# Performance work log

Measured on AMD Instinct MI355X. Metric: run time of the kernel, lower is better.

## Reference

```python
import jax, jax.numpy as jnp
import numpy as np

B, T, I, H = 128, 512, 512, 512


def setup_inputs() -> dict:
    key = jax.random.key(0)
    k1, k2, k3, k4, k5 = jax.random.split(key, 5)
    scale_x = 1.0 / np.sqrt(I)
    scale_h = 1.0 / np.sqrt(H)
    return {
        "x": jax.random.normal(k1, (B, T, I), dtype=jnp.float32),
        "h0": jax.random.normal(k2, (B, H), dtype=jnp.float32),
        "Wx": jax.random.normal(k3, (3 * H, I), dtype=jnp.float32) * scale_x,
        "bx": jax.random.normal(k4, (3 * H,), dtype=jnp.float32) * scale_x,
        "Wh": jax.random.normal(k5, (3 * H, H), dtype=jnp.float32) * scale_h,
    }


def reference(x, h0, Wx, bx, Wh):
    # Precompute input projections for all timesteps as one big GEMM:
    # [B,T,I] @ [I,3H] -> [B,T,3H]
    x_lin = jnp.einsum('bti,ki->btk', x, Wx) + bx
    x_lin_t = jnp.swapaxes(x_lin, 0, 1)  # [T,B,3H] time-major for scan

    def step(h, xl):
        h_lin = h @ Wh.T                          # [B,3H]
        x_z, x_r, x_n = jnp.split(xl, 3, axis=1)
        h_z, h_r, h_n = jnp.split(h_lin, 3, axis=1)
        z = jax.nn.sigmoid(x_z + h_z)
        r = jax.nn.sigmoid(x_r + h_r)
        n = jnp.tanh(x_n + r * h_n)
        h_new = (1.0 - z) * n + z * h
        return h_new, h_new

    h_final, ys = jax.lax.scan(step, h0, x_lin_t)  # ys: [T,B,H]
    y = jnp.swapaxes(ys, 0, 1)                      # [B,T,H]
    return (y, h_final)
```

## Files before the change

### kernel.cpp

```cpp
#include <hip/hip_runtime.h>
#include <hip/hip_bf16.h>

#define B_  128
#define T_  512
#define HID 512
#define NG  1536
#define CSTRIDE 16

#define GCNT(t)  ((t)*CSTRIDE)
#define FLAG0    (T_*CSTRIDE)
#define MEM0     (FLAG0 + 256*CSTRIDE)
#define INIT0    (MEM0 + 8*CSTRIDE)
#define SYNC_U32 (INIT0 + CSTRIDE)

typedef __attribute__((ext_vector_type(8))) short bf16x8;
typedef __attribute__((ext_vector_type(4))) float f32x4;
typedef unsigned int uint;
typedef unsigned short u16;

#define HROW 1024
#define HPAR 131072

__device__ __forceinline__ float bf2f(unsigned short h) {
  union { unsigned u; float f; } c; c.u = ((unsigned)h) << 16; return c.f;
}
__device__ __forceinline__ unsigned short f2bf_rn(float f) {
  union { float f; unsigned u; } c; c.f = f;
  return (unsigned short)((c.u + 0x7FFFu + ((c.u >> 16) & 1u)) >> 16);
}
__device__ __forceinline__ void split1(float f, short& hi, short& lo) {
  union { float f; unsigned u; } c; c.f = f;
  unsigned short h = (unsigned short)(c.u >> 16);
  float r = f - bf2f(h);
  hi = (short)h; lo = (short)f2bf_rn(r);
}
__device__ __forceinline__ void split8(float4 a, float4 b, bf16x8& hi, bf16x8& lo) {
  float v[8] = {a.x,a.y,a.z,a.w,b.x,b.y,b.z,b.w};
  #pragma unroll
  for (int i = 0; i < 8; ++i) { short h,l; split1(v[i],h,l); hi[i]=h; lo[i]=l; }
}

__device__ __forceinline__ uint aload_rlx(const uint* p) {
  return __hip_atomic_load(p, __ATOMIC_RELAXED, __HIP_MEMORY_SCOPE_AGENT);
}

__global__ void h0_pack(const float* __restrict__ h0, u16* __restrict__ hbuf) {
  int i = blockIdx.x * 256 + threadIdx.x;
  short hi, lo; split1(h0[i], hi, lo);
  u16* p = hbuf + HPAR + (i >> 9) * HROW + (i & 511);
  p[0]   = (u16)hi;
  p[512] = (u16)lo;
}

template<bool WSF32>
__global__ __launch_bounds__(256) void xlin_kernel(const float* __restrict__ x,
                                                   const float* __restrict__ Wx,
                                                   const float* __restrict__ bx,
                                                   void* __restrict__ xlin) {
  const int lane = threadIdx.x & 63;
  const int w    = threadIdx.x >> 6;
  const int wm   = w & 1, wn = w >> 1;
  const int quad = lane >> 4, l16 = lane & 15;
  const long m0  = (long)blockIdx.y * 128;
  const int  n0  = blockIdx.x * 128;

  f32x4 acc[4][4];
  #pragma unroll
  for (int i = 0; i < 4; ++i)
    #pragma unroll
    for (int j = 0; j < 4; ++j) acc[i][j] = (f32x4){0.f,0.f,0.f,0.f};

  for (int kk = 0; kk < 16; ++kk) {
    const int kq = kk*32 + quad*8;
    bf16x8 ahi[4], alo[4], bhi[4], blo[4];
    #pragma unroll
    for (int i = 0; i < 4; ++i) {
      const float* p = x + (m0 + wm*64 + i*16 + l16) * HID + kq;
      float4 f0 = ((const float4*)p)[0], f1 = ((const float4*)p)[1];
      split8(f0, f1, ahi[i], alo[i]);
      const float* q = Wx + (long)(n0 + wn*64 + i*16 + l16) * HID + kq;
      float4 g0 = ((const float4*)q)[0], g1 = ((const float4*)q)[1];
      split8(g0, g1, bhi[i], blo[i]);
    }
    #pragma unroll
    for (int i = 0; i < 4; ++i)
      #pragma unroll
      for (int j = 0; j < 4; ++j) {
        acc[i][j] = __builtin_amdgcn_mfma_f32_16x16x32_bf16(ahi[i], bhi[j], acc[i][j], 0, 0, 0);
        acc[i][j] = __builtin_amdgcn_mfma_f32_16x16x32_bf16(ahi[i], blo[j], acc[i][j], 0, 0, 0);
        acc[i][j] = __builtin_amdgcn_mfma_f32_16x16x32_bf16(alo[i], bhi[j], acc[i][j], 0, 0, 0);
      }
  }
  #pragma unroll
  for (int i = 0; i < 4; ++i) {
    #pragma unroll
    for (int j = 0; j < 4; ++j) {
      const int n = n0 + wn*64 + j*16 + l16;
      const float bias = bx[n];
      #pragma unroll
      for (int r = 0; r < 4; ++r) {
        const long m = m0 + wm*64 + i*16 + quad*4 + r;
        const float v = acc[i][j][r] + bias;
        if (WSF32) ((float*)xlin)[m * NG + n] = v;
        else       ((unsigned short*)xlin)[m * NG + n] = f2bf_rn(v);
      }
    }
  }
}

template<bool WSF32>
__global__ __launch_bounds__(256, 1) void gru_rec(const void* __restrict__ xlin,
                                                  const float* __restrict__ Wh,
                                                  u16* __restrict__ hbuf,
                                                  uint* __restrict__ sync,
                                                  float* __restrict__ out) {
  __shared__ float red[3][4][16][17];
  __shared__ int sh_xcd, sh_cb, sh_kc;
  __shared__ uint sh_fast;
  const int tid  = threadIdx.x;
  const int lane = tid & 63;
  const int w    = tid >> 6;
  const int quad = lane >> 4, l16 = lane & 15;

  if (tid == 0) {
    uint id;
    __asm__ volatile("s_getreg_b32 %0, hwreg(HW_REG_XCC_ID, 0, 32)" : "=s"(id));
    const int xcd = (int)(id & 7u);
    uint xr = __hip_atomic_fetch_add(&sync[MEM0 + xcd*CSTRIDE], 1u,
                                     __ATOMIC_RELAXED, __HIP_MEMORY_SCOPE_AGENT);
    uint* ic = &sync[INIT0];
    uint gr = __hip_atomic_fetch_add(ic, 1u, __ATOMIC_ACQ_REL, __HIP_MEMORY_SCOPE_AGENT);
    while (aload_rlx(ic) < 256u) __builtin_amdgcn_s_sleep(1);
    (void)__hip_atomic_load(ic, __ATOMIC_ACQUIRE, __HIP_MEMORY_SCOPE_AGENT);
    bool bal = true;
    #pragma unroll
    for (int x = 0; x < 8; ++x)
      bal = bal && (aload_rlx(&sync[MEM0 + x*CSTRIDE]) == 32u);
    sh_xcd  = xcd;
    sh_fast = bal ? 1u : 0u;
    sh_cb   = bal ? xcd     : (int)(gr >> 5);
    sh_kc   = bal ? (int)xr : (int)(gr & 31u);
  }
  __syncthreads();
  const int  xcd   = sh_xcd;
  const bool fastm = (sh_fast != 0u);
  const int  cb    = sh_cb;
  const int  kc    = sh_kc;

  bf16x8 Bhi[3][4], Blo[3][4];
  #pragma unroll
  for (int g = 0; g < 3; ++g)
    #pragma unroll
    for (int kk = 0; kk < 4; ++kk) {
      const float* p = Wh + (long)(g*HID + kc*16 + l16) * HID + w*128 + kk*32 + quad*8;
      float4 f0 = ((const float4*)p)[0], f1 = ((const float4*)p)[1];
      split8(f0, f1, Bhi[g][kk], Blo[g][kk]);
    }

  const int bb   = tid >> 4;
  const int kk_  = tid & 15;
  const int brow = cb*16 + bb;
  const int ncol = kc*16 + kk_;
  float* yout = out;
  float* hfin = out + (long)B_ * T_ * HID;

  const int fragoff = (cb*16 + l16)*HROW + w*128 + quad*8;
  const int hpoff   = brow*HROW + ncol;

  float xq[8][3];
  float yq[8];

  {
    const long base = (long)brow * T_;
    #pragma unroll
    for (int q = 0; q < 8; ++q) {
      if (WSF32) {
        const float* xp = (const float*)xlin + (base + q) * NG + ncol;
        xq[q][0] = xp[0]; xq[q][1] = xp[HID]; xq[q][2] = xp[2*HID];
      } else {
        const unsigned short* xp = (const unsigned short*)xlin + (base + q) * NG + ncol;
        xq[q][0] = bf2f(xp[0]); xq[q][1] = bf2f(xp[HID]); xq[q][2] = bf2f(xp[2*HID]);
      }
    }
  }

  for (int tb = 0; tb < T_/8; ++tb) {
    #pragma unroll
    for (int ts = 0; ts < 8; ++ts) {
      const int t = tb*8 + ts;
      const float xz = xq[ts][0], xr = xq[ts][1], xn = xq[ts][2];

      if (t > 0) {
        if (fastm) {
          const uint* fp = &sync[FLAG0 + (xcd*32 + (lane & 31))*CSTRIDE];
          while (!__all(aload_rlx(fp) >= (uint)t)) __builtin_amdgcn_s_sleep(1);
        } else {
          if (tid == 0) {
            uint* gp = &sync[GCNT(t-1)];
            while (aload_rlx(gp) < 256u) __builtin_amdgcn_s_sleep(1);
            (void)__hip_atomic_load(gp, __ATOMIC_ACQUIRE, __HIP_MEMORY_SCOPE_AGENT);
          }
          __syncthreads();
        }
      }

      const u16* rb = hbuf + ((t + 1) & 1) * HPAR;
      u16*       wb = hbuf + (t & 1)       * HPAR;

      const u16* hp_ = rb + fragoff;
      const u16* hpp = rb + hpoff;
      uint4 u0,u1,u2,u3,u4,u5,u6,u7; uint hu, lu;
      asm volatile(
        "global_load_dwordx4 %0, %10, off sc0\n\t"
        "global_load_dwordx4 %1, %10, off offset:64 sc0\n\t"
        "global_load_dwordx4 %2, %10, off offset:128 sc0\n\t"
        "global_load_dwordx4 %3, %10, off offset:192 sc0\n\t"
        "global_load_dwordx4 %4, %10, off offset:1024 sc0\n\t"
        "global_load_dwordx4 %5, %10, off offset:1088 sc0\n\t"
        "global_load_dwordx4 %6, %10, off offset:1152 sc0\n\t"
        "global_load_dwordx4 %7, %10, off offset:1216 sc0\n\t"
        "global_load_ushort %8, %11, off sc0\n\t"
        "global_load_ushort %9, %11, off offset:1024 sc0\n\t"
        "s_waitcnt vmcnt(0)"
        : "=&v"(u0), "=&v"(u1), "=&v"(u2), "=&v"(u3),
          "=&v"(u4), "=&v"(u5), "=&v"(u6), "=&v"(u7),
          "=&v"(hu), "=&v"(lu)
        : "v"(hp_), "v"(hpp)
        : "memory");

      f32x4 acc[3] = { (f32x4){0,0,0,0}, (f32x4){0,0,0,0}, (f32x4){0,0,0,0} };
      {
        const bf16x8 ah0 = *(const bf16x8*)&u0, al0 = *(const bf16x8*)&u4;
        const bf16x8 ah1 = *(const bf16x8*)&u1, al1 = *(const bf16x8*)&u5;
        const bf16x8 ah2 = *(const bf16x8*)&u2, al2 = *(const bf16x8*)&u6;
        const bf16x8 ah3 = *(const bf16x8*)&u3, al3 = *(const bf16x8*)&u7;
        const bf16x8 AH[4] = {ah0, ah1, ah2, ah3};
        const bf16x8 AL[4] = {al0, al1, al2, al3};
        #pragma unroll
        for (int kk = 0; kk < 4; ++kk) {
          #pragma unroll
          for (int g = 0; g < 3; ++g) {
            acc[g] = __builtin_amdgcn_mfma_f32_16x16x32_bf16(AH[kk], Bhi[g][kk], acc[g], 0, 0, 0);
            acc[g] = __builtin_amdgcn_mfma_f32_16x16x32_bf16(AH[kk], Blo[g][kk], acc[g], 0, 0, 0);
            acc[g] = __builtin_amdgcn_mfma_f32_16x16x32_bf16(AL[kk], Bhi[g][kk], acc[g], 0, 0, 0);
          }
        }
      }
      #pragma unroll
      for (int g = 0; g < 3; ++g)
        #pragma unroll
        for (int r = 0; r < 4; ++r)
          red[g][w][quad*4 + r][l16] = acc[g][r];

      const float hp = bf2f((unsigned short)hu) + bf2f((unsigned short)lu);

      __syncthreads();

      float az = 0.f, ar = 0.f, an = 0.f;
      #pragma unroll
      for (int ww = 0; ww < 4; ++ww) {
        az += red[0][ww][bb][kk_];
        ar += red[1][ww][bb][kk_];
        an += red[2][ww][bb][kk_];
      }
      const float z = 1.f / (1.f + __expf(-(az + xz)));
      const float r = 1.f / (1.f + __expf(-(ar + xr)));
      const float pre = xn + r * an;
      const float e2 = __expf(-2.f * pre);
      const float n = 2.f / (1.f + e2) - 1.f;
      const float hn = (1.f - z) * n + z * hp;
      yq[ts] = hn;

      if (t < T_ - 1) {
        short shi, slo; split1(hn, shi, slo);
        u16* wp = wb + hpoff;
        wp[0]   = (u16)shi;
        wp[512] = (u16)slo;
      } else {
        hfin[brow*HID + ncol] = hn;
      }

      __syncthreads();
      if (t < T_ - 1) {
        if (fastm) {
          if (tid == 0)
            sync[FLAG0 + (xcd*32 + kc)*CSTRIDE] = (uint)(t + 1);
        } else {
          if (tid == 0)
            __hip_atomic_fetch_add(&sync[GCNT(t)], 1u,
                                   __ATOMIC_RELEASE, __HIP_MEMORY_SCOPE_AGENT);
        }
      }

      if (ts == 7) {
        #pragma unroll
        for (int q = 0; q < 8; ++q)
          __builtin_nontemporal_store(yq[q],
              &yout[((long)brow * T_ + tb*8 + q) * HID + ncol]);
        if (tb + 1 < T_/8) {
          const long base = (long)brow * T_ + (tb + 1)*8;
          #pragma unroll
          for (int q = 0; q < 8; ++q) {
            if (WSF32) {
              const float* xp = (const float*)xlin + (base + q) * NG + ncol;
              xq[q][0] = xp[0]; xq[q][1] = xp[HID]; xq[q][2] = xp[2*HID];
            } else {
              const unsigned short* xp = (const unsigned short*)xlin + (base + q) * NG + ncol;
              xq[q][0] = bf2f(xp[0]); xq[q][1] = bf2f(xp[HID]); xq[q][2] = bf2f(xp[2*HID]);
            }
          }
        }
      }
    }
  }
}

extern "C" void kernel_launch(void* const* d_in, const int* in_sizes, int n_in,
                              void* d_out, int out_size, void* d_ws, size_t ws_size,
                              hipStream_t stream) {
  const float* x  = (const float*)d_in[0];
  const float* h0 = (const float*)d_in[1];
  const float* Wx = (const float*)d_in[2];
  const float* bx = (const float*)d_in[3];
  const float* Wh = (const float*)d_in[4];
  float* out = (float*)d_out;

  const size_t xlin_f32  = (size_t)B_ * T_ * NG * 4;
  const size_t xlin_bf16 = (size_t)B_ * T_ * NG * 2;
  const size_t hbuf_sz   = (size_t)2 * HPAR * 2;
  const size_t sync_sz   = (size_t)SYNC_U32 * 4;

  const bool wsf32 = (ws_size >= xlin_f32 + hbuf_sz + sync_sz);
  const size_t xsz = wsf32 ? xlin_f32 : xlin_bf16;
  void* xlin = d_ws;
  u16*  hbuf = (u16*)((char*)d_ws + xsz);
  uint* sync = (uint*)((char*)d_ws + xsz + hbuf_sz);

  hipMemsetAsync(sync, 0, sync_sz, stream);
  h0_pack<<<256, 256, 0, stream>>>(h0, hbuf);
  if (wsf32) {
    xlin_kernel<true ><<<dim3(12, 512), 256, 0, stream>>>(x, Wx, bx, xlin);
    gru_rec<true >    <<<256, 256, 0, stream>>>(xlin, Wh, hbuf, sync, out);
  } else {
    xlin_kernel<false><<<dim3(12, 512), 256, 0, stream>>>(x, Wx, bx, xlin);
    gru_rec<false>    <<<256, 256, 0, stream>>>(xlin, Wh, hbuf, sync, out);
  }
}
```

Measured before the change: 2.022 ms.

## Halve recurrent workgroups, each computing 32 hidden columns, spin without sleep

The persistent recurrent kernel now launches 128 workgroups instead of 256. Each one handles 32 hidden columns per batch tile instead of 16, holding twice as many Wh fragments in registers and issuing twice the MFMAs per step. Fewer participants means the per-step flag barrier waits on fewer producers, which is meant to cut synchronisation latency. The fast-path spin loop also drops s_sleep to poll more aggressively. The trade-off is more serial MFMA and gate work per workgroup per timestep, higher register pressure, and half the CUs left idle.

```diff
diff --git a/kernel.cpp b/kernel.cpp
--- a/kernel.cpp
+++ b/kernel.cpp
@@ -12,6 +12,9 @@
 #define MEM0     (FLAG0 + 256*CSTRIDE)
 #define INIT0    (MEM0 + 8*CSTRIDE)
 #define SYNC_U32 (INIT0 + CSTRIDE)
+
+#define NWG      128
+#define NWG_XCD  16
 
 typedef __attribute__((ext_vector_type(8))) short bf16x8;
 typedef __attribute__((ext_vector_type(4))) float f32x4;
@@ -114,7 +117,7 @@
                                                   u16* __restrict__ hbuf,
                                                   uint* __restrict__ sync,
                                                   float* __restrict__ out) {
-  __shared__ float red[3][4][16][17];
+  __shared__ float red[3][4][16][34];
   __shared__ int sh_xcd, sh_cb, sh_kc;
   __shared__ uint sh_fast;
   const int tid  = threadIdx.x;
@@ -130,16 +133,16 @@
                                      __ATOMIC_RELAXED, __HIP_MEMORY_SCOPE_AGENT);
     uint* ic = &sync[INIT0];
     uint gr = __hip_atomic_fetch_add(ic, 1u, __ATOMIC_ACQ_REL, __HIP_MEMORY_SCOPE_AGENT);
-    while (aload_rlx(ic) < 256u) __builtin_amdgcn_s_sleep(1);
+    while (aload_rlx(ic) < (uint)NWG) __builtin_amdgcn_s_sleep(1);
     (void)__hip_atomic_load(ic, __ATOMIC_ACQUIRE, __HIP_MEMORY_SCOPE_AGENT);
     bool bal = true;
     #pragma unroll
     for (int x = 0; x < 8; ++x)
-      bal = bal && (aload_rlx(&sync[MEM0 + x*CSTRIDE]) == 32u);
+      bal = bal && (aload_rlx(&sync[MEM0 + x*CSTRIDE]) == (uint)NWG_XCD);
     sh_xcd  = xcd;
     sh_fast = bal ? 1u : 0u;
-    sh_cb   = bal ? xcd     : (int)(gr >> 5);
-    sh_kc   = bal ? (int)xr : (int)(gr & 31u);
+    sh_cb   = bal ? xcd     : (int)(gr >> 4);
+    sh_kc   = bal ? (int)xr : (int)(gr & 15u);
   }
   __syncthreads();
   const int  xcd   = sh_xcd;
@@ -147,39 +150,43 @@
   const int  cb    = sh_cb;
   const int  kc    = sh_kc;
 
-  bf16x8 Bhi[3][4], Blo[3][4];
+  bf16x8 Bhi[3][2][4], Blo[3][2][4];
   #pragma unroll
   for (int g = 0; g < 3; ++g)
     #pragma unroll
-    for (int kk = 0; kk < 4; ++kk) {
-      const float* p = Wh + (long)(g*HID + kc*16 + l16) * HID + w*128 + kk*32 + quad*8;
-      float4 f0 = ((const float4*)p)[0], f1 = ((const float4*)p)[1];
-      split8(f0, f1, Bhi[g][kk], Blo[g][kk]);
-    }
-
-  const int bb   = tid >> 4;
-  const int kk_  = tid & 15;
-  const int brow = cb*16 + bb;
-  const int ncol = kc*16 + kk_;
+    for (int c = 0; c < 2; ++c)
+      #pragma unroll
+      for (int kk = 0; kk < 4; ++kk) {
+        const float* p = Wh + (long)(g*HID + kc*32 + c*16 + l16) * HID + w*128 + kk*32 + quad*8;
+        float4 f0 = ((const float4*)p)[0], f1 = ((const float4*)p)[1];
+        split8(f0, f1, Bhi[g][c][kk], Blo[g][c][kk]);
+      }
+
+  const int bb    = tid >> 4;
+  const int kk2   = tid & 15;
+  const int brow  = cb*16 + bb;
+  const int ncol0 = kc*32 + kk2;
   float* yout = out;
   float* hfin = out + (long)B_ * T_ * HID;
 
   const int fragoff = (cb*16 + l16)*HROW + w*128 + quad*8;
-  const int hpoff   = brow*HROW + ncol;
-
-  float xq[8][3];
-  float yq[8];
+  const int hpoff   = brow*HROW + ncol0;
+
+  float xq[8][6];
+  float yq[8][2];
 
   {
     const long base = (long)brow * T_;
     #pragma unroll
     for (int q = 0; q < 8; ++q) {
       if (WSF32) {
-        const float* xp = (const float*)xlin + (base + q) * NG + ncol;
-        xq[q][0] = xp[0]; xq[q][1] = xp[HID]; xq[q][2] = xp[2*HID];
+        const float* xp = (const float*)xlin + (base + q) * NG + ncol0;
+        xq[q][0] = xp[0];  xq[q][1] = xp[HID];    xq[q][2] = xp[2*HID];
+        xq[q][3] = xp[16]; xq[q][4] = xp[HID+16]; xq[q][5] = xp[2*HID+16];
       } else {
-        const unsigned short* xp = (const unsigned short*)xlin + (base + q) * NG + ncol;
-        xq[q][0] = bf2f(xp[0]); xq[q][1] = bf2f(xp[HID]); xq[q][2] = bf2f(xp[2*HID]);
+        const unsigned short* xp = (const unsigned short*)xlin + (base + q) * NG + ncol0;
+        xq[q][0] = bf2f(xp[0]);  xq[q][1] = bf2f(xp[HID]);    xq[q][2] = bf2f(xp[2*HID]);
+        xq[q][3] = bf2f(xp[16]); xq[q][4] = bf2f(xp[HID+16]); xq[q][5] = bf2f(xp[2*HID+16]);
       }
     }
   }
@@ -188,16 +195,15 @@
     #pragma unroll
     for (int ts = 0; ts < 8; ++ts) {
       const int t = tb*8 + ts;
-      const float xz = xq[ts][0], xr = xq[ts][1], xn = xq[ts][2];
 
       if (t > 0) {
         if (fastm) {
-          const uint* fp = &sync[FLAG0 + (xcd*32 + (lane & 31))*CSTRIDE];
-          while (!__all(aload_rlx(fp) >= (uint)t)) __builtin_amdgcn_s_sleep(1);
+          const uint* fp = &sync[FLAG0 + (xcd*16 + (lane & 15))*CSTRIDE];
+          while (!__all(aload_rlx(fp) >= (uint)t)) { }
         } else {
           if (tid == 0) {
             uint* gp = &sync[GCNT(t-1)];
-            while (aload_rlx(gp) < 256u) __builtin_amdgcn_s_sleep(1);
+            while (aload_rlx(gp) < (uint)NWG) __builtin_amdgcn_s_sleep(1);
             (void)__hip_atomic_load(gp, __ATOMIC_ACQUIRE, __HIP_MEMORY_SCOPE_AGENT);
           }
           __syncthreads();
@@ -209,82 +215,97 @@
 
       const u16* hp_ = rb + fragoff;
       const u16* hpp = rb + hpoff;
-      uint4 u0,u1,u2,u3,u4,u5,u6,u7; uint hu, lu;
+      uint4 u0,u1,u2,u3,u4,u5,u6,u7; uint hu0, hu1, lu0, lu1;
       asm volatile(
-        "global_load_dwordx4 %0, %10, off sc0\n\t"
-        "global_load_dwordx4 %1, %10, off offset:64 sc0\n\t"
-        "global_load_dwordx4 %2, %10, off offset:128 sc0\n\t"
-        "global_load_dwordx4 %3, %10, off offset:192 sc0\n\t"
-        "global_load_dwordx4 %4, %10, off offset:1024 sc0\n\t"
-        "global_load_dwordx4 %5, %10, off offset:1088 sc0\n\t"
-        "global_load_dwordx4 %6, %10, off offset:1152 sc0\n\t"
-        "global_load_dwordx4 %7, %10, off offset:1216 sc0\n\t"
-        "global_load_ushort %8, %11, off sc0\n\t"
-        "global_load_ushort %9, %11, off offset:1024 sc0\n\t"
+        "global_load_dwordx4 %0, %12, off sc0\n\t"
+        "global_load_dwordx4 %1, %12, off offset:64 sc0\n\t"
+        "global_load_dwordx4 %2, %12, off offset:128 sc0\n\t"
+        "global_load_dwordx4 %3, %12, off offset:192 sc0\n\t"
+        "global_load_dwordx4 %4, %12, off offset:1024 sc0\n\t"
+        "global_load_dwordx4 %5, %12, off offset:1088 sc0\n\t"
+        "global_load_dwordx4 %6, %12, off offset:1152 sc0\n\t"
+        "global_load_dwordx4 %7, %12, off offset:1216 sc0\n\t"
+        "global_load_ushort %8, %13, off sc0\n\t"
+        "global_load_ushort %9, %13, off offset:32 sc0\n\t"
+        "global_load_ushort %10, %13, off offset:1024 sc0\n\t"
+        "global_load_ushort %11, %13, off offset:1056 sc0\n\t"
         "s_waitcnt vmcnt(0)"
         : "=&v"(u0), "=&v"(u1), "=&v"(u2), "=&v"(u3),
           "=&v"(u4), "=&v"(u5), "=&v"(u6), "=&v"(u7),
-          "=&v"(hu), "=&v"(lu)
+          "=&v"(hu0), "=&v"(hu1), "=&v"(lu0), "=&v"(lu1)
         : "v"(hp_), "v"(hpp)
         : "memory");
 
-      f32x4 acc[3] = { (f32x4){0,0,0,0}, (f32x4){0,0,0,0}, (f32x4){0,0,0,0} };
+      f32x4 acc[3][2];
+      #pragma unroll
+      for (int g = 0; g < 3; ++g)
+        #pragma unroll
+        for (int c = 0; c < 2; ++c) acc[g][c] = (f32x4){0,0,0,0};
       {
-        const bf16x8 ah0 = *(const bf16x8*)&u0, al0 = *(const bf16x8*)&u4;
-        const bf16x8 ah1 = *(const bf16x8*)&u1, al1 = *(const bf16x8*)&u5;
-        const bf16x8 ah2 = *(const bf16x8*)&u2, al2 = *(const bf16x8*)&u6;
-        const bf16x8 ah3 = *(const bf16x8*)&u3, al3 = *(const bf16x8*)&u7;
-        const bf16x8 AH[4] = {ah0, ah1, ah2, ah3};
-        const bf16x8 AL[4] = {al0, al1, al2, al3};
+        const bf16x8 AH[4] = { *(const bf16x8*)&u0, *(const bf16x8*)&u1,
+                               *(const bf16x8*)&u2, *(const bf16x8*)&u3 };
+        const bf16x8 AL[4] = { *(const bf16x8*)&u4, *(const bf16x8*)&u5,
+                               *(const bf16x8*)&u6, *(const bf16x8*)&u7 };
         #pragma unroll
         for (int kk = 0; kk < 4; ++kk) {
           #pragma unroll
           for (int g = 0; g < 3; ++g) {
-            acc[g] = __builtin_amdgcn_mfma_f32_16x16x32_bf16(AH[kk], Bhi[g][kk], acc[g], 0, 0, 0);
-            acc[g] = __builtin_amdgcn_mfma_f32_16x16x32_bf16(AH[kk], Blo[g][kk], acc[g], 0, 0, 0);
-            acc[g] = __builtin_amdgcn_mfma_f32_16x16x32_bf16(AL[kk], Bhi[g][kk], acc[g], 0, 0, 0);
+            #pragma unroll
+            for (int c = 0; c < 2; ++c) {
+              acc[g][c] = __builtin_amdgcn_mfma_f32_16x16x32_bf16(AH[kk], Bhi[g][c][kk], acc[g][c], 0, 0, 0);
+              acc[g][c] = __builtin_amdgcn_mfma_f32_16x16x32_bf16(AH[kk], Blo[g][c][kk], acc[g][c], 0, 0, 0);
+              acc[g][c] = __builtin_amdgcn_mfma_f32_16x16x32_bf16(AL[kk], Bhi[g][c][kk], acc[g][c], 0, 0, 0);
+            }
           }
         }
       }
       #pragma unroll
       for (int g = 0; g < 3; ++g)
         #pragma unroll
-        for (int r = 0; r < 4; ++r)
-          red[g][w][quad*4 + r][l16] = acc[g][r];
-
-      const float hp = bf2f((unsigned short)hu) + bf2f((unsigned short)lu);
+        for (int c = 0; c < 2; ++c)
+          #pragma unroll
+          for (int r = 0; r < 4; ++r)
+            red[g][w][quad*4 + r][c*16 + l16] = acc[g][c][r];
+
+      const float hp0 = bf2f((unsigned short)hu0) + bf2f((unsigned short)lu0);
+      const float hp1 = bf2f((unsigned short)hu1) + bf2f((unsigned short)lu1);
 
       __syncthreads();
 
-      float az = 0.f, ar = 0.f, an = 0.f;
+      float az0=0.f, ar0=0.f, an0=0.f, az1=0.f, ar1=0.f, an1=0.f;
       #pragma unroll
       for (int ww = 0; ww < 4; ++ww) {
-        az += red[0][ww][bb][kk_];
-        ar += red[1][ww][bb][kk_];
-        an += red[2][ww][bb][kk_];
-      }
-      const float z = 1.f / (1.f + __expf(-(az + xz)));
-      const float r = 1.f / (1.f + __expf(-(ar + xr)));
-      const float pre = xn + r * an;
-      const float e2 = __expf(-2.f * pre);
-      const float n = 2.f / (1.f + e2) - 1.f;
-      const float hn = (1.f - z) * n + z * hp;
-      yq[ts] = hn;
+        az0 += red[0][ww][bb][kk2];      az1 += red[0][ww][bb][16+kk2];
+        ar0 += red[1][ww][bb][kk2];      ar1 += red[1][ww][bb][16+kk2];
+        an0 += red[2][ww][bb][kk2];      an1 += red[2][ww][bb][16+kk2];
+      }
+      const float z0 = 1.f / (1.f + __expf(-(az0 + xq[ts][0])));
+      const float r0 = 1.f / (1.f + __expf(-(ar0 + xq[ts][1])));
+      const float p0 = xq[ts][2] + r0 * an0;
+      const float n0 = 2.f / (1.f + __expf(-2.f * p0)) - 1.f;
+      const float hn0 = (1.f - z0) * n0 + z0 * hp0;
+      const float z1 = 1.f / (1.f + __expf(-(az1 + xq[ts][3])));
+      const float r1 = 1.f / (1.f + __expf(-(ar1 + xq[ts][4])));
+      const float p1 = xq[ts][5] + r1 * an1;
+      const float n1 = 2.f / (1.f + __expf(-2.f * p1)) - 1.f;
+      const float hn1 = (1.f - z1) * n1 + z1 * hp1;
+      yq[ts][0] = hn0; yq[ts][1] = hn1;
 
       if (t < T_ - 1) {
-        short shi, slo; split1(hn, shi, slo);
+        short h0h,h0l,h1h,h1l; split1(hn0,h0h,h0l); split1(hn1,h1h,h1l);
         u16* wp = wb + hpoff;
-        wp[0]   = (u16)shi;
-        wp[512] = (u16)slo;
+        wp[0]   = (u16)h0h;  wp[16]  = (u16)h1h;
+        wp[512] = (u16)h0l;  wp[528] = (u16)h1l;
       } else {
-        hfin[brow*HID + ncol] = hn;
+        hfin[brow*HID + ncol0]      = hn0;
+        hfin[brow*HID + ncol0 + 16] = hn1;
       }
 
       __syncthreads();
       if (t < T_ - 1) {
         if (fastm) {
           if (tid == 0)
-            sync[FLAG0 + (xcd*32 + kc)*CSTRIDE] = (uint)(t + 1);
+            sync[FLAG0 + (xcd*16 + kc)*CSTRIDE] = (uint)(t + 1);
         } else {
           if (tid == 0)
             __hip_atomic_fetch_add(&sync[GCNT(t)], 1u,
@@ -294,19 +315,23 @@
 
       if (ts == 7) {
         #pragma unroll
-        for (int q = 0; q < 8; ++q)
-          __builtin_nontemporal_store(yq[q],
-              &yout[((long)brow * T_ + tb*8 + q) * HID + ncol]);
+        for (int q = 0; q < 8; ++q) {
+          float* yp = &yout[((long)brow * T_ + tb*8 + q) * HID + ncol0];
+          __builtin_nontemporal_store(yq[q][0], yp);
+          __builtin_nontemporal_store(yq[q][1], yp + 16);
+        }
         if (tb + 1 < T_/8) {
           const long base = (long)brow * T_ + (tb + 1)*8;
           #pragma unroll
           for (int q = 0; q < 8; ++q) {
             if (WSF32) {
-              const float* xp = (const float*)xlin + (base + q) * NG + ncol;
-              xq[q][0] = xp[0]; xq[q][1] = xp[HID]; xq[q][2] = xp[2*HID];
+              const float* xp = (const float*)xlin + (base + q) * NG + ncol0;
+              xq[q][0] = xp[0];  xq[q][1] = xp[HID];    xq[q][2] = xp[2*HID];
+              xq[q][3] = xp[16]; xq[q][4] = xp[HID+16]; xq[q][5] = xp[2*HID+16];
             } else {
-              const unsigned short* xp = (const unsigned short*)xlin + (base + q) * NG + ncol;
-              xq[q][0] = bf2f(xp[0]); xq[q][1] = bf2f(xp[HID]); xq[q][2] = bf2f(xp[2*HID]);
+              const unsigned short* xp = (const unsigned short*)xlin + (base + q) * NG + ncol0;
+              xq[q][0] = bf2f(xp[0]);  xq[q][1] = bf2f(xp[HID]);    xq[q][2] = bf2f(xp[2*HID]);
+              xq[q][3] = bf2f(xp[16]); xq[q][4] = bf2f(xp[HID+16]); xq[q][5] = bf2f(xp[2*HID+16]);
             }
           }
         }
@@ -340,9 +365,9 @@
   h0_pack<<<256, 256, 0, stream>>>(h0, hbuf);
   if (wsf32) {
     xlin_kernel<true ><<<dim3(12, 512), 256, 0, stream>>>(x, Wx, bx, xlin);
-    gru_rec<true >    <<<256, 256, 0, stream>>>(xlin, Wh, hbuf, sync, out);
+    gru_rec<true >    <<<NWG, 256, 0, stream>>>(xlin, Wh, hbuf, sync, out);
   } else {
     xlin_kernel<false><<<dim3(12, 512), 256, 0, stream>>>(x, Wx, bx, xlin);
-    gru_rec<false>    <<<256, 256, 0, stream>>>(xlin, Wh, hbuf, sync, out);
-  }
-}
+    gru_rec<false>    <<<NWG, 256, 0, stream>>>(xlin, Wh, hbuf, sync, out);
+  }
+}
```

Measured after the change: 2.332 ms. 15.3% more time.
